# Kernel tuning notes

Measured on AMD Instinct MI355X. Metric: run time of the kernel, lower is better.

Reference implementation:

```python
import jax, jax.numpy as jnp
import numpy as np

N = 50000          # nodes
E = 800000         # edges (avg degree 16)
IN, H, OUT = 128, 256, 128
K = 100            # low-rank attention rank (hard-coded self.k = 100)
BN_EPS = 1e-5


def _lin(key, din, dout):
    return jax.random.normal(key, (din, dout), jnp.float32) / np.sqrt(din)


def setup_inputs() -> dict:
    key = jax.random.key(0)
    ks = jax.random.split(key, 16)
    inp = {
        "x": jax.random.normal(ks[0], (N, IN), jnp.float32),
        "edge_index": jax.random.randint(ks[1], (2, E), 0, N, jnp.int32),
    }
    dins = [IN, H, H]
    douts = [H, H, OUT]
    j = 2
    for i, (di, do) in enumerate(zip(dins, douts)):
        inp[f"cw{i}"] = _lin(ks[j], di, H); j += 1          # GCNConv weight
        inp[f"cb{i}"] = jnp.zeros((H,), jnp.float32)          # GCNConv bias
        inp[f"aw{i}"] = _lin(ks[j], di, 4 * K); j += 1        # attention U|V|Z|T projection
        inp[f"ab{i}"] = jnp.zeros((4 * K,), jnp.float32)
        inp[f"rw{i}"] = _lin(ks[j], 2 * K + H, do); j += 1    # dimension_reduce linear
        inp[f"rb{i}"] = jnp.zeros((do,), jnp.float32)
    for i in range(2):                                        # BN for first num_layers-1 blocks
        inp[f"g{i}"] = jnp.ones((H,), jnp.float32)
        inp[f"bt{i}"] = jnp.zeros((H,), jnp.float32)
    return inp


def _gcn(x, W, b, src, dst):
    n = x.shape[0]
    loops = jnp.arange(n, dtype=src.dtype)
    s = jnp.concatenate([src, loops])
    d = jnp.concatenate([dst, loops])
    deg = jax.ops.segment_sum(jnp.ones(d.shape, x.dtype), d, num_segments=n)
    dis = jax.lax.rsqrt(jnp.maximum(deg, 1.0))  # deg >= 1 due to self loops
    h = x @ W                                    # [N, H]
    msg = h[s] * (dis[s] * dis[d])[:, None]      # [E+N, H]
    return jax.ops.segment_sum(msg, d, num_segments=n) + b


def _lowrank(x, Aw, Ab):
    # LowRankAttention: tmp = relu(x W); split into U,V,Z,T of width K each.
    t = jax.nn.relu(x @ Aw + Ab)                 # [N, 4K]
    U, V, Z, T = t[:, :K], t[:, K:2 * K], t[:, 2 * K:3 * K], t[:, 3 * K:]
    n = x.shape[0]
    # joint_normalize2: scalar norm factor
    nf = jnp.sum(U @ (V.T @ jnp.ones((n, 1), x.dtype))) / n + 1e-6
    res = U @ (V.T @ Z)                          # low-rank global attention [N, K]
    return jnp.concatenate([res / nf, T], axis=1)  # [N, 2K]


def _bn(x, g, b):
    m = jnp.mean(x, axis=0)
    v = jnp.var(x, axis=0)
    return (x - m) * jax.lax.rsqrt(v + BN_EPS) * g + b


def reference(x, edge_index, cw0, cb0, aw0, ab0, rw0, rb0, g0, bt0,
              cw1, cb1, aw1, ab1, rw1, rb1, g1, bt1,
              cw2, cb2, aw2, ab2, rw2, rb2):
    src, dst = edge_index[0], edge_index[1]
    layers = [(cw0, cb0, aw0, ab0, rw0, rb0, g0, bt0),
              (cw1, cb1, aw1, ab1, rw1, rb1, g1, bt1)]
    for cw, cb, aw, ab, rw, rb, g, bt in layers:
        x_local = jax.nn.relu(_gcn(x, cw, cb, src, dst))  # dropout p=0 (eval)
        x_global = _lowrank(x, aw, ab)
        x = jax.nn.relu(jnp.concatenate([x_global, x_local], axis=1) @ rw + rb)
        x = _bn(x, g, bt)
    x_local = jax.nn.relu(_gcn(x, cw2, cb2, src, dst))
    x_global = _lowrank(x, aw2, ab2)
    return jnp.concatenate([x_global, x_local], axis=1) @ rw2 + rb2
```

## Files before the change

### kernel.cpp

```cpp
#include <hip/hip_runtime.h>

typedef _Float16 f16;
typedef __attribute__((ext_vector_type(8))) _Float16 f16x8;
typedef __attribute__((ext_vector_type(4))) _Float16 f16x4;
typedef __attribute__((ext_vector_type(2))) _Float16 f16x2;
typedef __attribute__((ext_vector_type(4))) float f32x4;

#define BKMAX 256
#define LDB   264

__global__ __launch_bounds__(256) void gemm_mfma(
    const f16* __restrict__ A, int lda,
    const f16* __restrict__ Bt, int Kd,
    const float* __restrict__ bias,
    f16* __restrict__ Cb, float* __restrict__ Cf, int ldc,
    int R, int ncols, int relu,
    const float* __restrict__ scale_ptr)
{
    __shared__ f16 Bs[128 * LDB];
    const int tid  = threadIdx.x;
    const int wid  = tid >> 6;
    const int lane = tid & 63;
    const int m    = lane & 15;
    const int quad = lane >> 4;

    const long row0    = (long)blockIdx.x * 128 + wid * 32;
    const int  colbase = blockIdx.y * 128;

    f32x4 acc[2][8];
#pragma unroll
    for (int rt = 0; rt < 2; ++rt)
#pragma unroll
        for (int ct = 0; ct < 8; ++ct)
            acc[rt][ct] = f32x4{0.f, 0.f, 0.f, 0.f};

    const f16* Aptr[2];
#pragma unroll
    for (int rt = 0; rt < 2; ++rt) {
        long r = row0 + rt * 16 + m;
        if (r > (long)R - 1) r = (long)R - 1;
        Aptr[rt] = A + r * (long)lda + quad * 8;
    }

    f16x8 pa0 = *(const f16x8*)(Aptr[0]);
    f16x8 pa1 = *(const f16x8*)(Aptr[1]);

    const int  scol = tid >> 1;
    const int  shalf = (tid & 1) * 8;
    const long sbase = (long)(colbase + scol) * Kd;

    for (int k0 = 0; k0 < Kd; k0 += BKMAX) {
        const int BK = (Kd - k0 < BKMAX) ? (Kd - k0) : BKMAX;
        if (k0 != 0) __syncthreads();
        for (int kc = shalf; kc < BK; kc += 16)
            *(f16x8*)&Bs[scol * LDB + kc] = *(const f16x8*)(Bt + sbase + k0 + kc);
        __syncthreads();
#pragma unroll 2
        for (int kk = 0; kk < BK; kk += 32) {
            f16x8 a0 = pa0, a1 = pa1;
            int kn = k0 + kk + 32;
            if (kn < Kd) {
                pa0 = *(const f16x8*)(Aptr[0] + kn);
                pa1 = *(const f16x8*)(Aptr[1] + kn);
            }
#pragma unroll
            for (int ct = 0; ct < 8; ++ct) {
                f16x8 b = *(const f16x8*)&Bs[(ct * 16 + m) * LDB + kk + quad * 8];
                acc[0][ct] = __builtin_amdgcn_mfma_f32_16x16x32_f16(a0, b, acc[0][ct], 0, 0, 0);
                acc[1][ct] = __builtin_amdgcn_mfma_f32_16x16x32_f16(a1, b, acc[1][ct], 0, 0, 0);
            }
        }
    }

    const float scale = scale_ptr ? *scale_ptr : 1.f;
#pragma unroll
    for (int ct = 0; ct < 8; ++ct) {
        int col = colbase + ct * 16 + m;
        if (col >= ncols) continue;
        float bv = bias ? bias[col] : 0.f;
#pragma unroll
        for (int rt = 0; rt < 2; ++rt) {
#pragma unroll
            for (int r = 0; r < 4; ++r) {
                long row = row0 + rt * 16 + quad * 4 + r;
                if (row < R) {
                    float v = acc[rt][ct][r] * scale + bv;
                    if (relu && v < 0.f) v = 0.f;
                    if (Cf) Cf[row * (long)ldc + col] = v;
                    else    Cb[row * (long)ldc + col] = (f16)v;
                }
            }
        }
    }
}

__global__ __launch_bounds__(256, 2) void gemm_mfma_t(
    const f16* __restrict__ A, int lda,
    const f16* __restrict__ Bt, int Kd,
    const float* __restrict__ bias,
    f16* __restrict__ Cb, float* __restrict__ Cf, int ldc,
    int R, int ncols, int relu,
    const float* __restrict__ scale_ptr,
    float* __restrict__ colsum_ptr,
    float* __restrict__ bnsum_ptr)
{
    __shared__ f16 Bs[128 * LDB];
    const int tid  = threadIdx.x;
    const int wid  = tid >> 6;
    const int lane = tid & 63;
    const int m    = lane & 15;
    const int quad = lane >> 4;

    const long row0    = (long)blockIdx.x * 256 + wid * 64;
    const int  colbase = blockIdx.y * 128;

    f32x4 acc[4][8];
#pragma unroll
    for (int rt = 0; rt < 4; ++rt)
#pragma unroll
        for (int ct = 0; ct < 8; ++ct)
            acc[rt][ct] = f32x4{0.f, 0.f, 0.f, 0.f};

    const f16* Aptr[4];
#pragma unroll
    for (int rt = 0; rt < 4; ++rt) {
        long r = row0 + rt * 16 + m;
        if (r > (long)R - 1) r = (long)R - 1;
        Aptr[rt] = A + r * (long)lda + quad * 8;
    }

    f16x8 pa[4];
#pragma unroll
    for (int rt = 0; rt < 4; ++rt) pa[rt] = *(const f16x8*)(Aptr[rt]);

    const int  scol = tid >> 1;
    const int  shalf = (tid & 1) * 8;
    const long sbase = (long)(colbase + scol) * Kd;

    for (int k0 = 0; k0 < Kd; k0 += BKMAX) {
        const int BK = (Kd - k0 < BKMAX) ? (Kd - k0) : BKMAX;
        if (k0 != 0) __syncthreads();
        for (int kc = shalf; kc < BK; kc += 16)
            *(f16x8*)&Bs[scol * LDB + kc] = *(const f16x8*)(Bt + sbase + k0 + kc);
        __syncthreads();
#pragma unroll 2
        for (int kk = 0; kk < BK; kk += 32) {
            f16x8 a[4];
#pragma unroll
            for (int rt = 0; rt < 4; ++rt) a[rt] = pa[rt];
            int kn = k0 + kk + 32;
            if (kn < Kd) {
#pragma unroll
                for (int rt = 0; rt < 4; ++rt) pa[rt] = *(const f16x8*)(Aptr[rt] + kn);
            }
#pragma unroll
            for (int ct = 0; ct < 8; ++ct) {
                f16x8 b = *(const f16x8*)&Bs[(ct * 16 + m) * LDB + kk + quad * 8];
#pragma unroll
                for (int rt = 0; rt < 4; ++rt)
                    acc[rt][ct] = __builtin_amdgcn_mfma_f32_16x16x32_f16(a[rt], b, acc[rt][ct], 0, 0, 0);
            }
        }
    }

    const float scale = scale_ptr ? *scale_ptr : 1.f;
    float rsum[8], rsq[8];
#pragma unroll
    for (int ct = 0; ct < 8; ++ct) { rsum[ct] = 0.f; rsq[ct] = 0.f; }

#pragma unroll
    for (int ct = 0; ct < 8; ++ct) {
        int col = colbase + ct * 16 + m;
        if (col >= ncols) continue;
        float bv = bias ? bias[col] : 0.f;
#pragma unroll
        for (int rt = 0; rt < 4; ++rt) {
#pragma unroll
            for (int r = 0; r < 4; ++r) {
                long row = row0 + rt * 16 + quad * 4 + r;
                if (row < R) {
                    float v = acc[rt][ct][r] * scale + bv;
                    if (relu && v < 0.f) v = 0.f;
                    if (Cf) Cf[row * (long)ldc + col] = v;
                    else    Cb[row * (long)ldc + col] = (f16)v;
                    rsum[ct] += v;
                    rsq[ct]  += v * v;
                }
            }
        }
    }

    if (colsum_ptr || bnsum_ptr) {
        __syncthreads();
        float* scr = (float*)Bs;
#pragma unroll
        for (int ct = 0; ct < 8; ++ct) {
            float s = rsum[ct];
            s += __shfl_xor(s, 16);
            s += __shfl_xor(s, 32);
            float q = rsq[ct];
            q += __shfl_xor(q, 16);
            q += __shfl_xor(q, 32);
            if (quad == 0) {
                scr[wid * 128 + ct * 16 + m]       = s;
                scr[512 + wid * 128 + ct * 16 + m] = q;
            }
        }
        __syncthreads();
        if (tid < 128) {
            int col = colbase + tid;
            if (col < ncols) {
                float s = scr[tid] + scr[128 + tid] + scr[256 + tid] + scr[384 + tid];
                if (colsum_ptr && col < 200) atomicAdd(&colsum_ptr[col], s);
                if (bnsum_ptr) {
                    float q = scr[512 + tid] + scr[640 + tid] + scr[768 + tid] + scr[896 + tid];
                    atomicAdd(&bnsum_ptr[col], s);
                    atomicAdd(&bnsum_ptr[256 + col], q);
                }
            }
        }
    }
}

__global__ void transpose_f2b(const float* __restrict__ in, int K, int ncols,
                              f16* __restrict__ out, int Kd, int npad)
{
    long idx = (long)blockIdx.x * 256 + threadIdx.x;
    long total = (long)npad * Kd;
    if (idx >= total) return;
    int k = (int)(idx % Kd);
    int n = (int)(idx / Kd);
    float v = (k < K && n < ncols) ? in[(long)k * ncols + n] : 0.f;
    out[idx] = (f16)v;
}

__global__ void cast_f2b(const float* __restrict__ in, long total, f16* __restrict__ out)
{
    long idx = (long)blockIdx.x * 256 + threadIdx.x;
    if (idx < total) out[idx] = (f16)in[idx];
}

__global__ void hist_kernel(const int* __restrict__ dst, int E, int* __restrict__ cnt)
{
    int e = blockIdx.x * 256 + threadIdx.x;
    if (e < E) atomicAdd(&cnt[dst[e]], 1);
}

__global__ __launch_bounds__(1024) void scanA_kernel(const int* __restrict__ cnt, int n,
                                                     int* __restrict__ csum)
{
    __shared__ int sdata[1024];
    int t = threadIdx.x;
    int i = blockIdx.x * 1024 + t;
    sdata[t] = (i < n) ? cnt[i] : 0;
    __syncthreads();
    for (int d = 512; d > 0; d >>= 1) {
        if (t < d) sdata[t] += sdata[t + d];
        __syncthreads();
    }
    if (t == 0) csum[blockIdx.x] = sdata[0];
}

__global__ void scanB_kernel(int* __restrict__ csum, int nchunks, int n, int* __restrict__ rowptr)
{
    if (threadIdx.x == 0) {
        int run = 0;
        for (int b = 0; b < nchunks; ++b) {
            int v = csum[b];
            csum[b] = run;
            run += v;
        }
        rowptr[n] = run;
    }
}

__global__ __launch_bounds__(1024) void scanC_kernel(const int* __restrict__ cnt, int n,
                                                     const int* __restrict__ csum,
                                                     int* __restrict__ rowptr,
                                                     int* __restrict__ cursor,
                                                     float* __restrict__ dis)
{
    __shared__ int sdata[1024];
    int t = threadIdx.x;
    int i = blockIdx.x * 1024 + t;
    int v = (i < n) ? cnt[i] : 0;
    sdata[t] = v;
    __syncthreads();
    for (int d = 1; d < 1024; d <<= 1) {
        int x = (t >= d) ? sdata[t - d] : 0;
        __syncthreads();
        sdata[t] += x;
        __syncthreads();
    }
    if (i < n) {
        int excl = csum[blockIdx.x] + sdata[t] - v;
        rowptr[i] = excl;
        cursor[i] = excl;
        dis[i] = rsqrtf((float)(v + 1));
    }
}

__global__ void scatter_kernel(const int* __restrict__ src, const int* __restrict__ dst,
                               int E, int* __restrict__ cursor, int* __restrict__ colidx)
{
    int e = blockIdx.x * 256 + threadIdx.x;
    if (e < E) {
        int d = dst[e];
        int pos = atomicAdd(&cursor[d], 1);
        colidx[pos] = src[e];
    }
}

__global__ __launch_bounds__(256) void agg_kernel(
    const f16* __restrict__ h, const int* __restrict__ rowptr,
    const int* __restrict__ colidx, const float* __restrict__ dis,
    const float* __restrict__ cb, f16* __restrict__ out, int ldc, int R)
{
    int wid = threadIdx.x >> 6, lane = threadIdx.x & 63;
    int i = blockIdx.x * 4 + wid;
    if (i >= R) return;
    float disi = dis[i];
    f16x4 hv = *(const f16x4*)(h + (long)i * 256 + lane * 4);
    float acc[4];
#pragma unroll
    for (int j = 0; j < 4; ++j) acc[j] = (float)hv[j] * disi;
    int e0 = rowptr[i], e1 = rowptr[i + 1];
    int e = e0;
    for (; e + 3 < e1; e += 4) {
        int s0 = colidx[e], s1 = colidx[e + 1], s2 = colidx[e + 2], s3 = colidx[e + 3];
        float w0 = dis[s0], w1 = dis[s1], w2 = dis[s2], w3 = dis[s3];
        f16x4 h0 = *(const f16x4*)(h + (long)s0 * 256 + lane * 4);
        f16x4 h1 = *(const f16x4*)(h + (long)s1 * 256 + lane * 4);
        f16x4 h2 = *(const f16x4*)(h + (long)s2 * 256 + lane * 4);
        f16x4 h3 = *(const f16x4*)(h + (long)s3 * 256 + lane * 4);
#pragma unroll
        for (int j = 0; j < 4; ++j)
            acc[j] += (float)h0[j] * w0 + (float)h1[j] * w1
                    + (float)h2[j] * w2 + (float)h3[j] * w3;
    }
    for (; e < e1; ++e) {
        int s = colidx[e];
        float w = dis[s];
        f16x4 hs = *(const f16x4*)(h + (long)s * 256 + lane * 4);
#pragma unroll
        for (int j = 0; j < 4; ++j) acc[j] += (float)hs[j] * w;
    }
    f16x4 o;
#pragma unroll
    for (int j = 0; j < 4; ++j) {
        float v = acc[j] * disi + cb[lane * 4 + j];
        if (v < 0.f) v = 0.f;
        o[j] = (f16)v;
    }
    *(f16x4*)(out + (long)i * ldc + lane * 4) = o;
}

__global__ void nf_kernel(float* __restrict__ cs, float* __restrict__ scale, int R)
{
    __shared__ float s[128];
    int t = threadIdx.x;
    float v = 0.f;
    if (t < 100) {
        v = cs[t] * cs[100 + t];
        cs[t] = 0.f;
        cs[100 + t] = 0.f;
    }
    s[t] = v;
    __syncthreads();
    for (int d = 64; d > 0; d >>= 1) {
        if (t < d) s[t] += s[t + d];
        __syncthreads();
    }
    if (t == 0) scale[0] = 1.0f / (s[0] / (float)R + 1e-6f);
}

#define VTZ_BLOCKS 192
__global__ __launch_bounds__(256) void vtz_mfma(const f16* __restrict__ t, int ld, int R,
                                                float* __restrict__ Mpart)
{
    __shared__ f16 Vt[112 * 72];
    __shared__ f16 Zt[112 * 72];
    const int tid  = threadIdx.x;
    const int wid  = tid >> 6;
    const int lane = tid & 63;
    const int m    = lane & 15;
    const int quad = lane >> 4;

    for (int idx = tid; idx < 12 * 64; idx += 256) {
        int c = 100 + (idx >> 6), r = idx & 63;
        Vt[c * 72 + r] = (f16)0.f;
        Zt[c * 72 + r] = (f16)0.f;
    }

    f32x4 acc[2][7];
#pragma unroll
    for (int rt = 0; rt < 2; ++rt)
#pragma unroll
        for (int ct = 0; ct < 7; ++ct)
            acc[rt][ct] = f32x4{0.f, 0.f, 0.f, 0.f};

    for (long base = (long)blockIdx.x * 64; base < R; base += (long)gridDim.x * 64) {
        __syncthreads();
        for (int idx = tid; idx < 50 * 64; idx += 256) {
            int r = idx / 50, c2 = (idx - r * 50) * 2;
            f16x2 v2 = f16x2{(f16)0.f, (f16)0.f};
            f16x2 z2 = f16x2{(f16)0.f, (f16)0.f};
            if (base + r < R) {
                v2 = *(const f16x2*)(t + (base + r) * ld + 100 + c2);
                z2 = *(const f16x2*)(t + (base + r) * ld + 200 + c2);
            }
            Vt[c2 * 72 + r] = v2[0]; Vt[(c2 + 1) * 72 + r] = v2[1];
            Zt[c2 * 72 + r] = z2[0]; Zt[(c2 + 1) * 72 + r] = z2[1];
        }
        __syncthreads();
#pragma unroll
        for (int ks = 0; ks < 2; ++ks) {
            int k0 = ks * 32 + quad * 8;
            f16x8 b[7];
#pragma unroll
            for (int ct = 0; ct < 7; ++ct)
                b[ct] = *(const f16x8*)&Zt[(ct * 16 + m) * 72 + k0];
#pragma unroll
            for (int rt = 0; rt < 2; ++rt) {
                int tr = wid + rt * 4;
                if (tr >= 7) continue;
                f16x8 a = *(const f16x8*)&Vt[(tr * 16 + m) * 72 + k0];
#pragma unroll
                for (int ct = 0; ct < 7; ++ct)
                    acc[rt][ct] = __builtin_amdgcn_mfma_f32_16x16x32_f16(a, b[ct], acc[rt][ct], 0, 0, 0);
            }
        }
    }

    float* out = Mpart + (long)blockIdx.x * 10000;
#pragma unroll
    for (int rt = 0; rt < 2; ++rt) {
        int tr = wid + rt * 4;
        if (tr >= 7) continue;
#pragma unroll
        for (int ct = 0; ct < 7; ++ct) {
            int b = ct * 16 + m;
            if (b >= 100) continue;
#pragma unroll
            for (int r = 0; r < 4; ++r) {
                int a = tr * 16 + quad * 4 + r;
                if (a < 100) out[a * 100 + b] = acc[rt][ct][r];
            }
        }
    }
}

__global__ void vtz_reduce2(const float* __restrict__ Mpart, f16* __restrict__ MT,
                            const float* __restrict__ scale_ptr)
{
    int idx = blockIdx.x * 256 + threadIdx.x;
    if (idx >= 10000) return;
    float s = 0.f;
    for (int b = 0; b < VTZ_BLOCKS; ++b) s += Mpart[(long)b * 10000 + idx];
    s *= *scale_ptr;
    int a = idx / 100, c = idx - a * 100;
    MT[c * 128 + a] = (f16)s;
}

__global__ void bn_finalize(float* __restrict__ sums, const float* __restrict__ g,
                            const float* __restrict__ bt, int R, float* __restrict__ ab)
{
    int c = threadIdx.x;
    float s0 = sums[c];
    float s1 = sums[256 + c];
    sums[c] = 0.f;
    sums[256 + c] = 0.f;
    float mean = s0 / (float)R;
    float var  = s1 / (float)R - mean * mean;
    if (var < 0.f) var = 0.f;
    float a = g[c] * rsqrtf(var + 1e-5f);
    ab[c] = a;
    ab[256 + c] = bt[c] - mean * a;
}

__global__ __launch_bounds__(256) void bn_fold_all(
    f16* __restrict__ cwT, f16* __restrict__ awT,
    const float* __restrict__ cwf, const float* __restrict__ awf,
    const float* __restrict__ ab,
    const float* __restrict__ ab0,
    float* __restrict__ cb2, float* __restrict__ ab2)
{
    const int bid = blockIdx.x;
    const int t   = threadIdx.x;
    if (bid < 256) {
        int idx = bid * 256 + t;
        cwT[idx] = (f16)((float)cwT[idx] * ab[idx & 255]);
    } else if (bid < 768) {
        int idx = (bid - 256) * 256 + t;
        awT[idx] = (f16)((float)awT[idx] * ab[idx & 255]);
    } else if (bid == 768) {
        float s = 0.f;
        for (int k = 0; k < 256; ++k) s += ab[256 + k] * cwf[(long)k * 256 + t];
        cb2[t] = s;
    } else {
        int n = (bid - 769) * 256 + t;
        if (n < 400) {
            float s = ab0[n];
            for (int k = 0; k < 256; ++k) s += ab[256 + k] * awf[(long)k * 400 + n];
            ab2[n] = s;
        }
    }
}

extern "C" void kernel_launch(void* const* d_in, const int* in_sizes, int n_in,
                              void* d_out, int out_size, void* d_ws, size_t ws_size,
                              hipStream_t stream)
{
    (void)n_in; (void)out_size; (void)ws_size;
    const int N = in_sizes[0] / 128;
    const int E = in_sizes[1] / 2;

    const float* x0 = (const float*)d_in[0];
    const int*  ei   = (const int*)d_in[1];
    const int*  esrc = ei;
    const int*  edst = ei + E;
    const float *cw[3], *cbv[3], *aw[3], *abv[3], *rw[3], *rbv[3];
    for (int l = 0; l < 3; ++l) {
        cw[l]  = (const float*)d_in[2 + 6 * l];
        cbv[l] = (const float*)d_in[3 + 6 * l];
        aw[l]  = (const float*)d_in[4 + 6 * l];
        abv[l] = (const float*)d_in[5 + 6 * l];
        rw[l]  = (const float*)d_in[6 + 6 * l];
        rbv[l] = (const float*)d_in[7 + 6 * l];
    }
    const float* g[2]   = {(const float*)d_in[20], (const float*)d_in[22]};
    const float* btb[2] = {(const float*)d_in[21], (const float*)d_in[23]};

    char* p = (char*)d_ws;
    auto carve = [&](size_t bytes) -> char* {
        char* r = p; p += (bytes + 255) & ~(size_t)255; return r;
    };
    int*   cnt    = (int*)carve((size_t)N * 4);
    int*   rowptr = (int*)carve((size_t)(N + 1) * 4);
    int*   cursor = (int*)carve((size_t)N * 4);
    int*   colidx = (int*)carve((size_t)E * 4);
    float* dis    = (float*)carve((size_t)N * 4);
    int*   csum   = (int*)carve(256 * 4);
    float* Mpart  = (float*)carve((size_t)VTZ_BLOCKS * 10000 * 4);
    float* csbuf  = (float*)carve(200 * 4);
    float* scale  = (float*)carve(256);
    float* bnsum  = (float*)carve(512 * 4);
    float* bnab   = (float*)carve(512 * 4);
    float* cb2    = (float*)carve(256 * 4);
    float* ab2    = (float*)carve(400 * 4);
    f16*   MT     = (f16*)carve(128 * 128 * 2);
    f16*   cwT[3], *awT[3], *rwT[3];
    int din[3] = {128, 256, 256};
    int dou[3] = {256, 256, 128};
    for (int l = 0; l < 3; ++l) {
        cwT[l] = (f16*)carve((size_t)256 * din[l] * 2);
        awT[l] = (f16*)carve((size_t)512 * din[l] * 2);
        rwT[l] = (f16*)carve((size_t)dou[l] * 480 * 2);
    }
    f16*   xbf  = (f16*)carve((size_t)N * 256 * 2);
    float* hbuf = (float*)carve((size_t)N * 256 * 4);
    f16*   hb   = (f16*)hbuf;
    f16*   tbuf = (f16*)carve((size_t)N * 300 * 2);
    f16*   xcat = (f16*)carve(((size_t)N * 456 + 32) * 2);

    const int nchunks = (N + 1023) / 1024;
    hipMemsetAsync(cnt, 0, (size_t)N * 4, stream);
    hist_kernel<<<(E + 255) / 256, 256, 0, stream>>>(edst, E, cnt);
    scanA_kernel<<<nchunks, 1024, 0, stream>>>(cnt, N, csum);
    scanB_kernel<<<1, 64, 0, stream>>>(csum, nchunks, N, rowptr);
    scanC_kernel<<<nchunks, 1024, 0, stream>>>(cnt, N, csum, rowptr, cursor, dis);
    scatter_kernel<<<(E + 255) / 256, 256, 0, stream>>>(esrc, edst, E, cursor, colidx);

    for (int l = 0; l < 3; ++l) {
        transpose_f2b<<<((long)256 * din[l] + 255) / 256, 256, 0, stream>>>(
            cw[l], din[l], 256, cwT[l], din[l], 256);
        transpose_f2b<<<((long)512 * din[l] + 255) / 256, 256, 0, stream>>>(
            aw[l], din[l], 400, awT[l], din[l], 512);
        transpose_f2b<<<((long)dou[l] * 480 + 255) / 256, 256, 0, stream>>>(
            rw[l], 456, dou[l], rwT[l], 480, dou[l]);
    }
    cast_f2b<<<((long)N * 128 + 255) / 256, 256, 0, stream>>>(x0, (long)N * 128, xbf);
    hipMemsetAsync(csbuf, 0, 200 * 4, stream);
    hipMemsetAsync(bnsum, 0, 512 * 4, stream);
    hipMemsetAsync(MT, 0, 128 * 128 * 2, stream);

    int lda = 128;
    const unsigned gx  = (unsigned)((N + 127) / 128);
    const unsigned gx2 = (unsigned)((N + 255) / 256);

    for (int l = 0; l < 3; ++l) {
        const float* gemm1_bias = (l > 0) ? cb2 : nullptr;
        const float* gemm2_bias = (l > 0) ? ab2 : abv[0];
        const float* gemm3_bias = (l > 0) ? ab2 + 300 : abv[0] + 300;

        gemm_mfma_t<<<dim3(gx2, 2), 256, 0, stream>>>(xbf, lda, cwT[l], din[l], gemm1_bias,
                                                      hb, nullptr, 256, N, 256, 0, nullptr,
                                                      nullptr, nullptr);
        gemm_mfma_t<<<dim3(gx2, 3), 256, 0, stream>>>(xbf, lda, awT[l], din[l], gemm2_bias,
                                                      tbuf, nullptr, 300, N, 300, 1, nullptr,
                                                      csbuf, nullptr);
        gemm_mfma<<<dim3(gx, 1), 256, 0, stream>>>(xbf, lda, awT[l] + (long)300 * din[l], din[l],
                                                   gemm3_bias,
                                                   xcat + 100, nullptr, 456, N, 100, 1, nullptr);
        nf_kernel<<<1, 128, 0, stream>>>(csbuf, scale, N);
        vtz_mfma<<<VTZ_BLOCKS, 256, 0, stream>>>(tbuf, 300, N, Mpart);
        vtz_reduce2<<<40, 256, 0, stream>>>(Mpart, MT, scale);
        gemm_mfma<<<dim3(gx, 1), 256, 0, stream>>>(tbuf, 300, MT, 128, nullptr,
                                                   xcat, nullptr, 456, N, 100, 0, nullptr);
        agg_kernel<<<(N + 3) / 4, 256, 0, stream>>>(hb, rowptr, colidx, dis, cbv[l],
                                                    xcat + 200, 456, N);
        if (l < 2) {
            gemm_mfma_t<<<dim3(gx2, 2), 256, 0, stream>>>(xcat, 456, rwT[l], 480, rbv[l],
                                                          xbf, nullptr, 256, N, 256, 1, nullptr,
                                                          nullptr, bnsum);
            bn_finalize<<<1, 256, 0, stream>>>(bnsum, g[l], btb[l], N, bnab);
            bn_fold_all<<<771, 256, 0, stream>>>(cwT[l + 1], awT[l + 1], cw[l + 1], aw[l + 1],
                                                 bnab, abv[l + 1], cb2, ab2);
            lda = 256;
        } else {
            gemm_mfma<<<dim3(gx, 1), 256, 0, stream>>>(xcat, 456, rwT[l], 480, rbv[l],
                                                       nullptr, (float*)d_out, 128, N, 128, 0, nullptr);
        }
    }
}
```

Measured before the change: 1.031 ms.

## Fuse per-layer input GEMMs and batch setup kernels into single launches

The three projections of x (GCN weight, low-rank U|V|Z block, and T block) become one GEMM against a concatenated 768-column weight, writing to hb, tbuf and xcat by column range and accumulating column sums for the normaliser. Weight transposes, the input cast, memsets and bias init are merged into one job-table prep kernel. The nf and bn_finalize kernels are folded into vtz_reduce2 and bn_fold2, with per-layer zeroed accumulators replacing in-kernel resets. This cuts launch count and reads x once per layer instead of three times, at the cost of some wasted padded columns (656 of 768 used) and redundant per-block scale recomputation.

```diff
diff --git a/kernel.cpp b/kernel.cpp
--- a/kernel.cpp
+++ b/kernel.cpp
@@ -8,6 +8,121 @@
 
 #define BKMAX 256
 #define LDB   264
+
+__global__ __launch_bounds__(256, 2) void gemm_fused3(
+    const f16* __restrict__ A, int lda,
+    const f16* __restrict__ Bt, int Kd,
+    const float* __restrict__ biascat,
+    f16* __restrict__ hb, f16* __restrict__ tbuf, f16* __restrict__ xcatT,
+    int R, float* __restrict__ csbuf)
+{
+    __shared__ f16 Bs[128 * LDB];
+    const int tid  = threadIdx.x;
+    const int wid  = tid >> 6;
+    const int lane = tid & 63;
+    const int m    = lane & 15;
+    const int quad = lane >> 4;
+
+    const long row0    = (long)blockIdx.x * 256 + wid * 64;
+    const int  colbase = blockIdx.y * 128;
+
+    f32x4 acc[4][8];
+#pragma unroll
+    for (int rt = 0; rt < 4; ++rt)
+#pragma unroll
+        for (int ct = 0; ct < 8; ++ct)
+            acc[rt][ct] = f32x4{0.f, 0.f, 0.f, 0.f};
+
+    const f16* Aptr[4];
+#pragma unroll
+    for (int rt = 0; rt < 4; ++rt) {
+        long r = row0 + rt * 16 + m;
+        if (r > (long)R - 1) r = (long)R - 1;
+        Aptr[rt] = A + r * (long)lda + quad * 8;
+    }
+    f16x8 pa[4];
+#pragma unroll
+    for (int rt = 0; rt < 4; ++rt) pa[rt] = *(const f16x8*)(Aptr[rt]);
+
+    const int  scol  = tid >> 1;
+    const int  shalf = (tid & 1) * 8;
+    const long sbase = (long)(colbase + scol) * Kd;
+
+    for (int k0 = 0; k0 < Kd; k0 += BKMAX) {
+        const int BK = (Kd - k0 < BKMAX) ? (Kd - k0) : BKMAX;
+        if (k0 != 0) __syncthreads();
+        for (int kc = shalf; kc < BK; kc += 16)
+            *(f16x8*)&Bs[scol * LDB + kc] = *(const f16x8*)(Bt + sbase + k0 + kc);
+        __syncthreads();
+#pragma unroll 2
+        for (int kk = 0; kk < BK; kk += 32) {
+            f16x8 a[4];
+#pragma unroll
+            for (int rt = 0; rt < 4; ++rt) a[rt] = pa[rt];
+            int kn = k0 + kk + 32;
+            if (kn < Kd) {
+#pragma unroll
+                for (int rt = 0; rt < 4; ++rt) pa[rt] = *(const f16x8*)(Aptr[rt] + kn);
+            }
+#pragma unroll
+            for (int ct = 0; ct < 8; ++ct) {
+                f16x8 b = *(const f16x8*)&Bs[(ct * 16 + m) * LDB + kk + quad * 8];
+#pragma unroll
+                for (int rt = 0; rt < 4; ++rt)
+                    acc[rt][ct] = __builtin_amdgcn_mfma_f32_16x16x32_f16(a[rt], b, acc[rt][ct], 0, 0, 0);
+            }
+        }
+    }
+
+    float rsum[8];
+#pragma unroll
+    for (int ct = 0; ct < 8; ++ct) rsum[ct] = 0.f;
+
+#pragma unroll
+    for (int ct = 0; ct < 8; ++ct) {
+        int col = colbase + ct * 16 + m;
+        if (col >= 656) continue;
+        float bv = biascat[col];
+        bool isrelu = col >= 256;
+        f16* dst; int ldc2, c2;
+        if (col < 256)      { dst = hb;    ldc2 = 256; c2 = col; }
+        else if (col < 556) { dst = tbuf;  ldc2 = 300; c2 = col - 256; }
+        else                { dst = xcatT; ldc2 = 456; c2 = col - 556; }
+#pragma unroll
+        for (int rt = 0; rt < 4; ++rt) {
+#pragma unroll
+            for (int r = 0; r < 4; ++r) {
+                long row = row0 + rt * 16 + quad * 4 + r;
+                if (row < R) {
+                    float v = acc[rt][ct][r] + bv;
+                    if (isrelu && v < 0.f) v = 0.f;
+                    dst[row * (long)ldc2 + c2] = (f16)v;
+                    rsum[ct] += v;
+                }
+            }
+        }
+    }
+
+    if (colbase == 256 || colbase == 384) {
+        __syncthreads();
+        float* scr = (float*)Bs;
+#pragma unroll
+        for (int ct = 0; ct < 8; ++ct) {
+            float s = rsum[ct];
+            s += __shfl_xor(s, 16);
+            s += __shfl_xor(s, 32);
+            if (quad == 0) scr[wid * 128 + ct * 16 + m] = s;
+        }
+        __syncthreads();
+        if (tid < 128) {
+            int gcol = colbase + tid;
+            if (gcol < 456) {
+                float s = scr[tid] + scr[128 + tid] + scr[256 + tid] + scr[384 + tid];
+                atomicAdd(&csbuf[gcol - 256], s);
+            }
+        }
+    }
+}
 
 __global__ __launch_bounds__(256) void gemm_mfma(
     const f16* __restrict__ A, int lda,
@@ -41,11 +156,10 @@
         if (r > (long)R - 1) r = (long)R - 1;
         Aptr[rt] = A + r * (long)lda + quad * 8;
     }
-
     f16x8 pa0 = *(const f16x8*)(Aptr[0]);
     f16x8 pa1 = *(const f16x8*)(Aptr[1]);
 
-    const int  scol = tid >> 1;
+    const int  scol  = tid >> 1;
     const int  shalf = (tid & 1) * 8;
     const long sbase = (long)(colbase + scol) * Kd;
 
@@ -100,8 +214,6 @@
     const float* __restrict__ bias,
     f16* __restrict__ Cb, float* __restrict__ Cf, int ldc,
     int R, int ncols, int relu,
-    const float* __restrict__ scale_ptr,
-    float* __restrict__ colsum_ptr,
     float* __restrict__ bnsum_ptr)
 {
     __shared__ f16 Bs[128 * LDB];
@@ -128,12 +240,11 @@
         if (r > (long)R - 1) r = (long)R - 1;
         Aptr[rt] = A + r * (long)lda + quad * 8;
     }
-
     f16x8 pa[4];
 #pragma unroll
     for (int rt = 0; rt < 4; ++rt) pa[rt] = *(const f16x8*)(Aptr[rt]);
 
-    const int  scol = tid >> 1;
+    const int  scol  = tid >> 1;
     const int  shalf = (tid & 1) * 8;
     const long sbase = (long)(colbase + scol) * Kd;
 
@@ -163,7 +274,6 @@
         }
     }
 
-    const float scale = scale_ptr ? *scale_ptr : 1.f;
     float rsum[8], rsq[8];
 #pragma unroll
     for (int ct = 0; ct < 8; ++ct) { rsum[ct] = 0.f; rsq[ct] = 0.f; }
@@ -179,7 +289,7 @@
             for (int r = 0; r < 4; ++r) {
                 long row = row0 + rt * 16 + quad * 4 + r;
                 if (row < R) {
-                    float v = acc[rt][ct][r] * scale + bv;
+                    float v = acc[rt][ct][r] + bv;
                     if (relu && v < 0.f) v = 0.f;
                     if (Cf) Cf[row * (long)ldc + col] = v;
                     else    Cb[row * (long)ldc + col] = (f16)v;
@@ -190,7 +300,7 @@
         }
     }
 
-    if (colsum_ptr || bnsum_ptr) {
+    if (bnsum_ptr) {
         __syncthreads();
         float* scr = (float*)Bs;
 #pragma unroll
@@ -211,33 +321,45 @@
             int col = colbase + tid;
             if (col < ncols) {
                 float s = scr[tid] + scr[128 + tid] + scr[256 + tid] + scr[384 + tid];
-                if (colsum_ptr && col < 200) atomicAdd(&colsum_ptr[col], s);
-                if (bnsum_ptr) {
-                    float q = scr[512 + tid] + scr[640 + tid] + scr[768 + tid] + scr[896 + tid];
-                    atomicAdd(&bnsum_ptr[col], s);
-                    atomicAdd(&bnsum_ptr[256 + col], q);
-                }
-            }
-        }
-    }
-}
-
-__global__ void transpose_f2b(const float* __restrict__ in, int K, int ncols,
-                              f16* __restrict__ out, int Kd, int npad)
-{
-    long idx = (long)blockIdx.x * 256 + threadIdx.x;
-    long total = (long)npad * Kd;
-    if (idx >= total) return;
-    int k = (int)(idx % Kd);
-    int n = (int)(idx / Kd);
-    float v = (k < K && n < ncols) ? in[(long)k * ncols + n] : 0.f;
-    out[idx] = (f16)v;
-}
-
-__global__ void cast_f2b(const float* __restrict__ in, long total, f16* __restrict__ out)
-{
-    long idx = (long)blockIdx.x * 256 + threadIdx.x;
-    if (idx < total) out[idx] = (f16)in[idx];
+                float q = scr[512 + tid] + scr[640 + tid] + scr[768 + tid] + scr[896 + tid];
+                atomicAdd(&bnsum_ptr[col], s);
+                atomicAdd(&bnsum_ptr[256 + col], q);
+            }
+        }
+    }
+}
+
+struct PrepJobs {
+    const float* src[13];
+    void*        dst[13];
+    int   K[13], ncols[13], Kd[13], type[13];
+    long  start[13], elems[13];
+    int   njobs;
+};
+
+__global__ __launch_bounds__(256) void prep_all(PrepJobs J)
+{
+    long b = blockIdx.x;
+    int j = 0;
+    for (int i = 1; i < J.njobs; ++i)
+        if (b >= J.start[i]) j = i;
+    long idx = (b - J.start[j]) * 256 + threadIdx.x;
+    if (idx >= J.elems[j]) return;
+    int ty = J.type[j];
+    if (ty == 0) {
+        int Kd = J.Kd[j];
+        int k = (int)(idx % Kd);
+        long n = idx / Kd;
+        float v = (k < J.K[j] && n < J.ncols[j]) ? J.src[j][(long)k * J.ncols[j] + n] : 0.f;
+        ((f16*)J.dst[j])[idx] = (f16)v;
+    } else if (ty == 1) {
+        ((f16*)J.dst[j])[idx] = (f16)J.src[j][idx];
+    } else if (ty == 2) {
+        ((float*)J.dst[j])[idx] = 0.f;
+    } else {
+        float v = (idx >= 256 && idx < 656) ? J.src[j][idx - 256] : 0.f;
+        ((float*)J.dst[j])[idx] = v;
+    }
 }
 
 __global__ void hist_kernel(const int* __restrict__ dst, int E, int* __restrict__ cnt)
@@ -355,25 +477,6 @@
     *(f16x4*)(out + (long)i * ldc + lane * 4) = o;
 }
 
-__global__ void nf_kernel(float* __restrict__ cs, float* __restrict__ scale, int R)
-{
-    __shared__ float s[128];
-    int t = threadIdx.x;
-    float v = 0.f;
-    if (t < 100) {
-        v = cs[t] * cs[100 + t];
-        cs[t] = 0.f;
-        cs[100 + t] = 0.f;
-    }
-    s[t] = v;
-    __syncthreads();
-    for (int d = 64; d > 0; d >>= 1) {
-        if (t < d) s[t] += s[t + d];
-        __syncthreads();
-    }
-    if (t == 0) scale[0] = 1.0f / (s[0] / (float)R + 1e-6f);
-}
-
 #define VTZ_BLOCKS 192
 __global__ __launch_bounds__(256) void vtz_mfma(const f16* __restrict__ t, int ld, int R,
                                                 float* __restrict__ Mpart)
@@ -450,59 +553,64 @@
     }
 }
 
-__global__ void vtz_reduce2(const float* __restrict__ Mpart, f16* __restrict__ MT,
-                            const float* __restrict__ scale_ptr)
-{
-    int idx = blockIdx.x * 256 + threadIdx.x;
+__global__ __launch_bounds__(256) void vtz_reduce2(const float* __restrict__ Mpart,
+                                                   f16* __restrict__ MT,
+                                                   const float* __restrict__ cs, int R)
+{
+    __shared__ float s2[256];
+    int t = threadIdx.x;
+    float v = (t < 100) ? cs[t] * cs[100 + t] : 0.f;
+    s2[t] = v;
+    __syncthreads();
+    for (int d = 128; d > 0; d >>= 1) {
+        if (t < d) s2[t] += s2[t + d];
+        __syncthreads();
+    }
+    float scale = 1.0f / (s2[0] / (float)R + 1e-6f);
+
+    int idx = blockIdx.x * 256 + t;
     if (idx >= 10000) return;
     float s = 0.f;
     for (int b = 0; b < VTZ_BLOCKS; ++b) s += Mpart[(long)b * 10000 + idx];
-    s *= *scale_ptr;
+    s *= scale;
     int a = idx / 100, c = idx - a * 100;
     MT[c * 128 + a] = (f16)s;
 }
 
-__global__ void bn_finalize(float* __restrict__ sums, const float* __restrict__ g,
-                            const float* __restrict__ bt, int R, float* __restrict__ ab)
-{
-    int c = threadIdx.x;
-    float s0 = sums[c];
-    float s1 = sums[256 + c];
-    sums[c] = 0.f;
-    sums[256 + c] = 0.f;
-    float mean = s0 / (float)R;
-    float var  = s1 / (float)R - mean * mean;
-    if (var < 0.f) var = 0.f;
-    float a = g[c] * rsqrtf(var + 1e-5f);
-    ab[c] = a;
-    ab[256 + c] = bt[c] - mean * a;
-}
-
-__global__ __launch_bounds__(256) void bn_fold_all(
-    f16* __restrict__ cwT, f16* __restrict__ awT,
+__global__ __launch_bounds__(256) void bn_fold2(
+    f16* __restrict__ bigBT,
     const float* __restrict__ cwf, const float* __restrict__ awf,
-    const float* __restrict__ ab,
-    const float* __restrict__ ab0,
-    float* __restrict__ cb2, float* __restrict__ ab2)
-{
+    const float* __restrict__ bnsum, const float* __restrict__ g,
+    const float* __restrict__ bt, int R,
+    const float* __restrict__ ab0, float* __restrict__ biascat)
+{
+    __shared__ float a_s[256], b_s[256];
+    const int t = threadIdx.x;
+    {
+        float s0 = bnsum[t];
+        float s1 = bnsum[256 + t];
+        float mean = s0 / (float)R;
+        float var  = s1 / (float)R - mean * mean;
+        if (var < 0.f) var = 0.f;
+        float a = g[t] * rsqrtf(var + 1e-5f);
+        a_s[t] = a;
+        b_s[t] = bt[t] - mean * a;
+    }
+    __syncthreads();
     const int bid = blockIdx.x;
-    const int t   = threadIdx.x;
-    if (bid < 256) {
-        int idx = bid * 256 + t;
-        cwT[idx] = (f16)((float)cwT[idx] * ab[idx & 255]);
-    } else if (bid < 768) {
-        int idx = (bid - 256) * 256 + t;
-        awT[idx] = (f16)((float)awT[idx] * ab[idx & 255]);
+    if (bid < 768) {
+        long idx = (long)bid * 256 + t;
+        bigBT[idx] = (f16)((float)bigBT[idx] * a_s[t]);
     } else if (bid == 768) {
         float s = 0.f;
-        for (int k = 0; k < 256; ++k) s += ab[256 + k] * cwf[(long)k * 256 + t];
-        cb2[t] = s;
+        for (int k = 0; k < 256; ++k) s += b_s[k] * cwf[(long)k * 256 + t];
+        biascat[t] = s;
     } else {
         int n = (bid - 769) * 256 + t;
         if (n < 400) {
             float s = ab0[n];
-            for (int k = 0; k < 256; ++k) s += ab[256 + k] * awf[(long)k * 400 + n];
-            ab2[n] = s;
+            for (int k = 0; k < 256; ++k) s += b_s[k] * awf[(long)k * 400 + n];
+            biascat[256 + n] = s;
         }
     }
 }
@@ -542,20 +650,18 @@
     float* dis    = (float*)carve((size_t)N * 4);
     int*   csum   = (int*)carve(256 * 4);
     float* Mpart  = (float*)carve((size_t)VTZ_BLOCKS * 10000 * 4);
-    float* csbuf  = (float*)carve(200 * 4);
-    float* scale  = (float*)carve(256);
-    float* bnsum  = (float*)carve(512 * 4);
-    float* bnab   = (float*)carve(512 * 4);
-    float* cb2    = (float*)carve(256 * 4);
-    float* ab2    = (float*)carve(400 * 4);
-    f16*   MT     = (f16*)carve(128 * 128 * 2);
-    f16*   cwT[3], *awT[3], *rwT[3];
+    float* zr     = (float*)carve(9984 * 4);
+    float* csbufL[3] = {zr, zr + 256, zr + 512};
+    float* bnsumA = zr + 768;
+    float* bnsumB = zr + 1280;
+    f16*   MT     = (f16*)(zr + 1792);
+    float* biascat = (float*)carve(768 * 4);
+    f16*   bigBT[3], *rwT[3];
     int din[3] = {128, 256, 256};
     int dou[3] = {256, 256, 128};
     for (int l = 0; l < 3; ++l) {
-        cwT[l] = (f16*)carve((size_t)256 * din[l] * 2);
-        awT[l] = (f16*)carve((size_t)512 * din[l] * 2);
-        rwT[l] = (f16*)carve((size_t)dou[l] * 480 * 2);
+        bigBT[l] = (f16*)carve((size_t)768 * din[l] * 2);
+        rwT[l]   = (f16*)carve((size_t)dou[l] * 480 * 2);
     }
     f16*   xbf  = (f16*)carve((size_t)N * 256 * 2);
     float* hbuf = (float*)carve((size_t)N * 256 * 4);
@@ -563,59 +669,56 @@
     f16*   tbuf = (f16*)carve((size_t)N * 300 * 2);
     f16*   xcat = (f16*)carve(((size_t)N * 456 + 32) * 2);
 
+    PrepJobs J{};
+    int nj = 0; long blk = 0;
+    auto addJob = [&](const float* s, void* d, int K, int nc, int Kd, int ty, long elems) {
+        J.src[nj] = s; J.dst[nj] = d; J.K[nj] = K; J.ncols[nj] = nc; J.Kd[nj] = Kd;
+        J.type[nj] = ty; J.start[nj] = blk; J.elems[nj] = elems;
+        blk += (elems + 255) / 256; ++nj;
+    };
+    for (int l = 0; l < 3; ++l)
+        addJob(cw[l], bigBT[l], din[l], 256, din[l], 0, (long)256 * din[l]);
+    for (int l = 0; l < 3; ++l)
+        addJob(aw[l], bigBT[l] + (long)256 * din[l], din[l], 400, din[l], 0, (long)512 * din[l]);
+    for (int l = 0; l < 3; ++l)
+        addJob(rw[l], rwT[l], 456, dou[l], 480, 0, (long)dou[l] * 480);
+    addJob(x0, xbf, 0, 0, 0, 1, (long)N * 128);
+    addJob(nullptr, zr, 0, 0, 0, 2, 9984);
+    addJob(nullptr, cnt, 0, 0, 0, 2, N);
+    addJob(abv[0], biascat, 0, 0, 0, 3, 768);
+    J.njobs = nj;
+
+    prep_all<<<(unsigned)blk, 256, 0, stream>>>(J);
+
     const int nchunks = (N + 1023) / 1024;
-    hipMemsetAsync(cnt, 0, (size_t)N * 4, stream);
     hist_kernel<<<(E + 255) / 256, 256, 0, stream>>>(edst, E, cnt);
     scanA_kernel<<<nchunks, 1024, 0, stream>>>(cnt, N, csum);
     scanB_kernel<<<1, 64, 0, stream>>>(csum, nchunks, N, rowptr);
     scanC_kernel<<<nchunks, 1024, 0, stream>>>(cnt, N, csum, rowptr, cursor, dis);
     scatter_kernel<<<(E + 255) / 256, 256, 0, stream>>>(esrc, edst, E, cursor, colidx);
 
-    for (int l = 0; l < 3; ++l) {
-        transpose_f2b<<<((long)256 * din[l] + 255) / 256, 256, 0, stream>>>(
-            cw[l], din[l], 256, cwT[l], din[l], 256);
-        transpose_f2b<<<((long)512 * din[l] + 255) / 256, 256, 0, stream>>>(
-            aw[l], din[l], 400, awT[l], din[l], 512);
-        transpose_f2b<<<((long)dou[l] * 480 + 255) / 256, 256, 0, stream>>>(
-            rw[l], 456, dou[l], rwT[l], 480, dou[l]);
-    }
-    cast_f2b<<<((long)N * 128 + 255) / 256, 256, 0, stream>>>(x0, (long)N * 128, xbf);
-    hipMemsetAsync(csbuf, 0, 200 * 4, stream);
-    hipMemsetAsync(bnsum, 0, 512 * 4, stream);
-    hipMemsetAsync(MT, 0, 128 * 128 * 2, stream);
-
     int lda = 128;
     const unsigned gx  = (unsigned)((N + 127) / 128);
     const unsigned gx2 = (unsigned)((N + 255) / 256);
 
     for (int l = 0; l < 3; ++l) {
-        const float* gemm1_bias = (l > 0) ? cb2 : nullptr;
-        const float* gemm2_bias = (l > 0) ? ab2 : abv[0];
-        const float* gemm3_bias = (l > 0) ? ab2 + 300 : abv[0] + 300;
-
-        gemm_mfma_t<<<dim3(gx2, 2), 256, 0, stream>>>(xbf, lda, cwT[l], din[l], gemm1_bias,
-                                                      hb, nullptr, 256, N, 256, 0, nullptr,
-                                                      nullptr, nullptr);
-        gemm_mfma_t<<<dim3(gx2, 3), 256, 0, stream>>>(xbf, lda, awT[l], din[l], gemm2_bias,
-                                                      tbuf, nullptr, 300, N, 300, 1, nullptr,
-                                                      csbuf, nullptr);
-        gemm_mfma<<<dim3(gx, 1), 256, 0, stream>>>(xbf, lda, awT[l] + (long)300 * din[l], din[l],
-                                                   gemm3_bias,
-                                                   xcat + 100, nullptr, 456, N, 100, 1, nullptr);
-        nf_kernel<<<1, 128, 0, stream>>>(csbuf, scale, N);
+        float* bnsumX = (l == 0) ? bnsumA : bnsumB;
+
+        gemm_fused3<<<dim3(gx2, 6), 256, 0, stream>>>(xbf, lda, bigBT[l], din[l], biascat,
+                                                      hb, tbuf, xcat + 100, N, csbufL[l]);
         vtz_mfma<<<VTZ_BLOCKS, 256, 0, stream>>>(tbuf, 300, N, Mpart);
-        vtz_reduce2<<<40, 256, 0, stream>>>(Mpart, MT, scale);
+        vtz_reduce2<<<40, 256, 0, stream>>>(Mpart, MT, csbufL[l], N);
         gemm_mfma<<<dim3(gx, 1), 256, 0, stream>>>(tbuf, 300, MT, 128, nullptr,
                                                    xcat, nullptr, 456, N, 100, 0, nullptr);
         agg_kernel<<<(N + 3) / 4, 256, 0, stream>>>(hb, rowptr, colidx, dis, cbv[l],
                                                     xcat + 200, 456, N);
         if (l < 2) {
             gemm_mfma_t<<<dim3(gx2, 2), 256, 0, stream>>>(xcat, 456, rwT[l], 480, rbv[l],
-                                                          xbf, nullptr, 256, N, 256, 1, nullptr,
-                                                          nullptr, bnsum);
-            bn_finalize<<<1, 256, 0, stream>>>(bnsum, g[l], btb[l], N, bnab);
-            bn_fold_all<<<771, 256, 0, stream>>>(cwT[l + 1], awT[l + 1], cw[l + 1], aw[l + 1],
-                                                 bnab, abv[l + 1], cb2, ab2);
+                                                          xbf, nullptr, 256, N, 256, 1,
+                                                          bnsumX);
+            bn_fold2<<<771, 256, 0, stream>>>(bigBT[l + 1], cw[l + 1], aw[l + 1],
+                                              bnsumX, g[l], btb[l], N,
+                                              abv[l + 1], biascat);
             lda = 256;
         } else {
             gemm_mfma<<<dim3(gx, 1), 256, 0, stream>>>(xcat, 456, rwT[l], 480, rbv[l],
```

After: 957.6 us. -7.1%, faster.
